# Performance work log

Hardware: AMD Instinct MI355X
Metric: run time of the kernel (lower is better)

The kernel has to match this reference:

```python
import jax, jax.numpy as jnp
import numpy as np

QMIN, QMAX = -128.0, 127.0  # int8 range

def setup_inputs() -> dict:
    key = jax.random.key(0)
    k1, k2 = jax.random.split(key)
    B, S, D_IN, D_OUT = 4, 2048, 4096, 4096
    x = jax.random.normal(k1, (B, S, D_IN), dtype=jnp.float32)
    # int8 weight stored as int32 (values in int8 range)
    weight = jax.random.randint(k2, (D_OUT, D_IN), -128, 128, dtype=jnp.int32)
    scale = jnp.array([0.02], dtype=jnp.float32)        # per-tensor weight scale
    input_scale = jnp.array([0.05], dtype=jnp.float32)  # static activation scale
    return {"x": x, "weight": weight, "scale": scale, "input_scale": input_scale}

def reference(x, weight, scale, input_scale):
    # quantize_static_quant_activations: round(x/input_scale) clamped to int8 range,
    # then direct_cast_dequantize back to fp32 (kept as fp32 here; values are integral).
    x_q = jnp.clip(jnp.round(x / input_scale), QMIN, QMAX)
    # direct_cast_dequantize(weight) -> fp32
    w = weight.astype(jnp.float32)
    # F.linear: x_q @ w.T  -> [B, S, D_OUT]
    out = jnp.einsum('bsi,oi->bso', x_q, w)
    # scale_dequantize with combined scale = input_scale * weight_scale
    return out * (input_scale * scale)
```

## Files before the change

### kernel.cpp

```cpp
#include <hip/hip_runtime.h>
#include <stdint.h>

typedef int v4i __attribute__((ext_vector_type(4)));

static constexpr int MDIM = 8192;
static constexpr int NDIM = 4096;
static constexpr int KDIM = 4096;
static constexpr int BM = 128;
static constexpr int BN = 128;
static constexpr int BK = 64;

__device__ __forceinline__ void lds_load16(const void* gptr, void* lptr) {
    __builtin_amdgcn_global_load_lds(
        (const __attribute__((address_space(1))) void*)(uintptr_t)gptr,
        (__attribute__((address_space(3))) void*)(uint32_t)(uintptr_t)lptr,
        16, 0, 0);
}

__global__ __launch_bounds__(256) void quant_x_k(const float4* __restrict__ x,
                                                 int* __restrict__ xq,
                                                 const float* __restrict__ s_in) {
    const int i = blockIdx.x * 256 + threadIdx.x;
    const float s = s_in[0];
    float4 v = x[i];
    const int q0 = (int)fminf(fmaxf(__builtin_rintf(v.x / s), -128.0f), 127.0f);
    const int q1 = (int)fminf(fmaxf(__builtin_rintf(v.y / s), -128.0f), 127.0f);
    const int q2 = (int)fminf(fmaxf(__builtin_rintf(v.z / s), -128.0f), 127.0f);
    const int q3 = (int)fminf(fmaxf(__builtin_rintf(v.w / s), -128.0f), 127.0f);
    xq[i] = (q0 & 0xff) | ((q1 & 0xff) << 8) | ((q2 & 0xff) << 16) | ((q3 & 0xff) << 24);
}

__global__ __launch_bounds__(256) void pack_w_k(const int4* __restrict__ w,
                                                int* __restrict__ wq) {
    const int i = blockIdx.x * 256 + threadIdx.x;
    int4 v = w[i];
    wq[i] = (v.x & 0xff) | ((v.y & 0xff) << 8) | ((v.z & 0xff) << 16) | ((v.w & 0xff) << 24);
}

__global__ __launch_bounds__(256) void gemm_i8_k(const int8_t* __restrict__ A,
                                                 const int8_t* __restrict__ Bt,
                                                 float* __restrict__ C,
                                                 const float* __restrict__ w_scale,
                                                 const float* __restrict__ in_scale) {
    __shared__ int8_t sA[BM * BK];
    __shared__ int8_t sB[BN * BK];

    const int tid  = threadIdx.x;
    const int lane = tid & 63;
    const int wave = tid >> 6;
    const int bm = blockIdx.y;
    const int bn = blockIdx.x;

    const int wm = (wave >> 1) * 64;
    const int wn = (wave & 1) * 64;
    const int lm = lane & 15;
    const int kq = (lane >> 4) * 16;

    v4i acc[4][4] = {};

    const int srow = tid >> 2;
    const int scol = (tid & 3) * 16;
    const int8_t* gA0 = A  + (size_t)(bm * BM + srow) * KDIM + scol;
    const int8_t* gB0 = Bt + (size_t)(bn * BN + srow) * KDIM + scol;
    const size_t half = (size_t)64 * KDIM;
    int8_t* lA0 = sA + wave * 1024;
    int8_t* lA1 = sA + 4096 + wave * 1024;
    int8_t* lB0 = sB + wave * 1024;
    int8_t* lB1 = sB + 4096 + wave * 1024;

    int aoff[4], boff[4];
#pragma unroll
    for (int t = 0; t < 4; ++t) {
        aoff[t] = (wm + t * 16 + lm) * BK + kq;
        boff[t] = (wn + t * 16 + lm) * BK + kq;
    }

    for (int k0 = 0; k0 < KDIM; k0 += BK) {
        __syncthreads();
        lds_load16(gA0 + k0,        lA0);
        lds_load16(gA0 + half + k0, lA1);
        lds_load16(gB0 + k0,        lB0);
        lds_load16(gB0 + half + k0, lB1);
        __syncthreads();

        v4i av[4], bv[4];
#pragma unroll
        for (int t = 0; t < 4; ++t) {
            av[t] = *(const v4i*)(sA + aoff[t]);
            bv[t] = *(const v4i*)(sB + boff[t]);
        }
#pragma unroll
        for (int mt = 0; mt < 4; ++mt)
#pragma unroll
            for (int nt = 0; nt < 4; ++nt)
                acc[mt][nt] = __builtin_amdgcn_mfma_i32_16x16x64_i8(
                    av[mt], bv[nt], acc[mt][nt], 0, 0, 0);
    }

    const float fs = w_scale[0] * in_scale[0];
    const int crow = (lane >> 4) * 4;
#pragma unroll
    for (int mt = 0; mt < 4; ++mt) {
#pragma unroll
        for (int nt = 0; nt < 4; ++nt) {
            const size_t n = (size_t)bn * BN + wn + nt * 16 + lm;
            const size_t mb = (size_t)bm * BM + wm + mt * 16 + crow;
#pragma unroll
            for (int r = 0; r < 4; ++r) {
                C[(mb + r) * NDIM + n] = (float)acc[mt][nt][r] * fs;
            }
        }
    }
}

extern "C" void kernel_launch(void* const* d_in, const int* in_sizes, int n_in,
                              void* d_out, int out_size, void* d_ws, size_t ws_size,
                              hipStream_t stream) {
    const float* x        = (const float*)d_in[0];
    const int*   w        = (const int*)d_in[1];
    const float* w_scale  = (const float*)d_in[2];
    const float* in_scale = (const float*)d_in[3];
    float* out = (float*)d_out;

    int8_t* xq = (int8_t*)d_ws;
    int8_t* wq = xq + (size_t)MDIM * KDIM;

    quant_x_k<<<(MDIM * KDIM / 4) / 256, 256, 0, stream>>>(
        (const float4*)x, (int*)xq, in_scale);
    pack_w_k<<<(NDIM * KDIM / 4) / 256, 256, 0, stream>>>(
        (const int4*)w, (int*)wq);

    dim3 grid(NDIM / BN, MDIM / BM);
    gemm_i8_k<<<grid, 256, 0, stream>>>(xq, wq, out, w_scale, in_scale);
}
```

Measured before the change: 413.0 us.

## Double GEMM K tile with XOR-swizzled LDS and merge prep kernels

The GEMM K tile grows from 64 to 128, so each barrier pair now covers two MFMA k-steps and the main loop has half as many synchronisations. LDS rows are stored with an XOR swizzle to avoid bank conflicts on the 128-byte row stride. The activation quantisation and weight packing kernels are merged into one launch, with each thread handling 16 elements and writing int4. In exchange, shared memory per block doubles, which may lower occupancy.

```diff
diff --git a/kernel.cpp b/kernel.cpp
--- a/kernel.cpp
+++ b/kernel.cpp
@@ -8,7 +8,10 @@
 static constexpr int KDIM = 4096;
 static constexpr int BM = 128;
 static constexpr int BN = 128;
-static constexpr int BK = 64;
+static constexpr int BK = 128;
+
+static constexpr int QBLOCKS = (MDIM * KDIM / 16) / 256;
+static constexpr int WBLOCKS = (NDIM * KDIM / 16) / 256;
 
 __device__ __forceinline__ void lds_load16(const void* gptr, void* lptr) {
     __builtin_amdgcn_global_load_lds(
@@ -17,24 +20,45 @@
         16, 0, 0);
 }
 
-__global__ __launch_bounds__(256) void quant_x_k(const float4* __restrict__ x,
-                                                 int* __restrict__ xq,
-                                                 const float* __restrict__ s_in) {
-    const int i = blockIdx.x * 256 + threadIdx.x;
-    const float s = s_in[0];
-    float4 v = x[i];
-    const int q0 = (int)fminf(fmaxf(__builtin_rintf(v.x / s), -128.0f), 127.0f);
-    const int q1 = (int)fminf(fmaxf(__builtin_rintf(v.y / s), -128.0f), 127.0f);
-    const int q2 = (int)fminf(fmaxf(__builtin_rintf(v.z / s), -128.0f), 127.0f);
-    const int q3 = (int)fminf(fmaxf(__builtin_rintf(v.w / s), -128.0f), 127.0f);
-    xq[i] = (q0 & 0xff) | ((q1 & 0xff) << 8) | ((q2 & 0xff) << 16) | ((q3 & 0xff) << 24);
+__device__ __forceinline__ int q1(float f, float s) {
+    return (int)fminf(fmaxf(__builtin_rintf(f / s), -128.0f), 127.0f);
+}
+__device__ __forceinline__ int pack4(int a, int b, int c, int d) {
+    return (a & 0xff) | ((b & 0xff) << 8) | ((c & 0xff) << 16) | ((d & 0xff) << 24);
 }
 
-__global__ __launch_bounds__(256) void pack_w_k(const int4* __restrict__ w,
-                                                int* __restrict__ wq) {
-    const int i = blockIdx.x * 256 + threadIdx.x;
-    int4 v = w[i];
-    wq[i] = (v.x & 0xff) | ((v.y & 0xff) << 8) | ((v.z & 0xff) << 16) | ((v.w & 0xff) << 24);
+__global__ __launch_bounds__(256) void prep_k(const float4* __restrict__ x,
+                                              int4* __restrict__ xq,
+                                              const int4* __restrict__ w,
+                                              int4* __restrict__ wq,
+                                              const float* __restrict__ s_in) {
+    const int b = blockIdx.x;
+    if (b < QBLOCKS) {
+        const int i = b * 256 + threadIdx.x;
+        const float s = s_in[0];
+        const float4 v0 = x[4 * i + 0];
+        const float4 v1 = x[4 * i + 1];
+        const float4 v2 = x[4 * i + 2];
+        const float4 v3 = x[4 * i + 3];
+        int4 o;
+        o.x = pack4(q1(v0.x, s), q1(v0.y, s), q1(v0.z, s), q1(v0.w, s));
+        o.y = pack4(q1(v1.x, s), q1(v1.y, s), q1(v1.z, s), q1(v1.w, s));
+        o.z = pack4(q1(v2.x, s), q1(v2.y, s), q1(v2.z, s), q1(v2.w, s));
+        o.w = pack4(q1(v3.x, s), q1(v3.y, s), q1(v3.z, s), q1(v3.w, s));
+        xq[i] = o;
+    } else {
+        const int i = (b - QBLOCKS) * 256 + threadIdx.x;
+        const int4 a = w[4 * i + 0];
+        const int4 c = w[4 * i + 1];
+        const int4 d = w[4 * i + 2];
+        const int4 e = w[4 * i + 3];
+        int4 o;
+        o.x = pack4(a.x, a.y, a.z, a.w);
+        o.y = pack4(c.x, c.y, c.z, c.w);
+        o.z = pack4(d.x, d.y, d.z, d.w);
+        o.w = pack4(e.x, e.y, e.z, e.w);
+        wq[i] = o;
+    }
 }
 
 __global__ __launch_bounds__(256) void gemm_i8_k(const int8_t* __restrict__ A,
@@ -54,56 +78,60 @@
     const int wm = (wave >> 1) * 64;
     const int wn = (wave & 1) * 64;
     const int lm = lane & 15;
-    const int kq = (lane >> 4) * 16;
+    const int q  = lane >> 4;
 
     v4i acc[4][4] = {};
 
-    const int srow = tid >> 2;
-    const int scol = (tid & 3) * 16;
-    const int8_t* gA0 = A  + (size_t)(bm * BM + srow) * KDIM + scol;
-    const int8_t* gB0 = Bt + (size_t)(bn * BN + srow) * KDIM + scol;
-    const size_t half = (size_t)64 * KDIM;
-    int8_t* lA0 = sA + wave * 1024;
-    int8_t* lA1 = sA + 4096 + wave * 1024;
-    int8_t* lB0 = sB + wave * 1024;
-    int8_t* lB1 = sB + 4096 + wave * 1024;
+    const int rr = wave * 32 + (lane >> 3);
+    const int cc = ((lane & 7) ^ (lane >> 3)) * 16;
+    const int8_t* gA0 = A  + (size_t)(bm * BM + rr) * KDIM + cc;
+    const int8_t* gB0 = Bt + (size_t)(bn * BN + rr) * KDIM + cc;
+    int8_t* lA0 = sA + wave * 4096;
+    int8_t* lB0 = sB + wave * 4096;
 
-    int aoff[4], boff[4];
+    int aoff[2][4], boff[2][4];
 #pragma unroll
-    for (int t = 0; t < 4; ++t) {
-        aoff[t] = (wm + t * 16 + lm) * BK + kq;
-        boff[t] = (wn + t * 16 + lm) * BK + kq;
-    }
+    for (int ks = 0; ks < 2; ++ks)
+#pragma unroll
+        for (int t = 0; t < 4; ++t) {
+            const int sw = (((ks * 4 + q) ^ (lm & 7)) << 4);
+            aoff[ks][t] = (wm + t * 16 + lm) * BK + sw;
+            boff[ks][t] = (wn + t * 16 + lm) * BK + sw;
+        }
 
     for (int k0 = 0; k0 < KDIM; k0 += BK) {
         __syncthreads();
-        lds_load16(gA0 + k0,        lA0);
-        lds_load16(gA0 + half + k0, lA1);
-        lds_load16(gB0 + k0,        lB0);
-        lds_load16(gB0 + half + k0, lB1);
+#pragma unroll
+        for (int j = 0; j < 4; ++j) {
+            lds_load16(gA0 + k0 + (size_t)j * (8 * KDIM), lA0 + j * 1024);
+            lds_load16(gB0 + k0 + (size_t)j * (8 * KDIM), lB0 + j * 1024);
+        }
         __syncthreads();
 
-        v4i av[4], bv[4];
 #pragma unroll
-        for (int t = 0; t < 4; ++t) {
-            av[t] = *(const v4i*)(sA + aoff[t]);
-            bv[t] = *(const v4i*)(sB + boff[t]);
+        for (int ks = 0; ks < 2; ++ks) {
+            v4i av[4], bv[4];
+#pragma unroll
+            for (int t = 0; t < 4; ++t) {
+                av[t] = *(const v4i*)(sA + aoff[ks][t]);
+                bv[t] = *(const v4i*)(sB + boff[ks][t]);
+            }
+#pragma unroll
+            for (int mt = 0; mt < 4; ++mt)
+#pragma unroll
+                for (int nt = 0; nt < 4; ++nt)
+                    acc[mt][nt] = __builtin_amdgcn_mfma_i32_16x16x64_i8(
+                        av[mt], bv[nt], acc[mt][nt], 0, 0, 0);
         }
-#pragma unroll
-        for (int mt = 0; mt < 4; ++mt)
-#pragma unroll
-            for (int nt = 0; nt < 4; ++nt)
-                acc[mt][nt] = __builtin_amdgcn_mfma_i32_16x16x64_i8(
-                    av[mt], bv[nt], acc[mt][nt], 0, 0, 0);
     }
 
     const float fs = w_scale[0] * in_scale[0];
-    const int crow = (lane >> 4) * 4;
+    const int crow = q * 4;
 #pragma unroll
     for (int mt = 0; mt < 4; ++mt) {
 #pragma unroll
         for (int nt = 0; nt < 4; ++nt) {
-            const size_t n = (size_t)bn * BN + wn + nt * 16 + lm;
+            const size_t n  = (size_t)bn * BN + wn + nt * 16 + lm;
             const size_t mb = (size_t)bm * BM + wm + mt * 16 + crow;
 #pragma unroll
             for (int r = 0; r < 4; ++r) {
@@ -125,10 +153,8 @@
     int8_t* xq = (int8_t*)d_ws;
     int8_t* wq = xq + (size_t)MDIM * KDIM;
 
-    quant_x_k<<<(MDIM * KDIM / 4) / 256, 256, 0, stream>>>(
-        (const float4*)x, (int*)xq, in_scale);
-    pack_w_k<<<(NDIM * KDIM / 4) / 256, 256, 0, stream>>>(
-        (const int4*)w, (int*)wq);
+    prep_k<<<QBLOCKS + WBLOCKS, 256, 0, stream>>>(
+        (const float4*)x, (int4*)xq, (const int4*)w, (int4*)wq, in_scale);
 
     dim3 grid(NDIM / BN, MDIM / BM);
     gemm_i8_k<<<grid, 256, 0, stream>>>(xq, wq, out, w_scale, in_scale);
```

Result: faster. 389.3 us (-5.8%).
